# Performance work log

Hardware: AMD Instinct MI355X
Metric: run time of the kernel (lower is better)

The kernel has to match this reference:

```python
import jax, jax.numpy as jnp
import numpy as np
from jax.scipy.special import logsumexp

B, T, S, V = 64, 1024, 512, 1024


def setup_inputs() -> dict:
    key = jax.random.key(0)
    k_obs, k_emis, k_trans, k_prior = jax.random.split(key, 4)
    observations = jax.random.randint(k_obs, (B, T), 0, V, dtype=jnp.int32)
    emission_table = jax.random.normal(k_emis, (V, S), dtype=jnp.float32)
    transitions = jax.random.normal(k_trans, (S, S), dtype=jnp.float32)
    prior = jax.random.normal(k_prior, (S,), dtype=jnp.float32)
    return {
        "observations": observations,
        "emission_table": emission_table,
        "transitions": transitions,
        "prior": prior,
    }


def reference(observations, emission_table, transitions, prior):
    # alpha_0[b, s] = emission_logits(obs_0)[b, s] + prior[s]
    alpha0 = emission_table[observations[:, 0]] + prior  # [B, S]

    def step(alpha, obs_t):
        # new_alpha[b, j] = emis[b, j] + logsumexp_i(alpha[b, i] + trans[i, j])
        e = emission_table[obs_t]  # [B, S]
        a = e + logsumexp(alpha[:, :, None] + transitions[None, :, :], axis=1)
        return a, None

    # scan over time steps 1..T-1; xs is [T-1, B]
    alpha, _ = jax.lax.scan(step, alpha0, observations[:, 1:].T)
    return logsumexp(alpha, axis=1)  # [B]
```

## Files before the change

kernel.cpp:

```cpp
#include <hip/hip_runtime.h>


constexpr int Bn = 64, Tn = 1024, Sn = 512;
#define L2E 1.44269504f

typedef int v4i __attribute__((ext_vector_type(4)));

#if __has_builtin(__builtin_amdgcn_update_dpp)
template <int CTRL>
__device__ __forceinline__ float dpp_fmax(float x) {
    int s = __builtin_bit_cast(int, x);
    int d = __builtin_amdgcn_update_dpp(s, s, CTRL, 0xf, 0xf, false);
    return fmaxf(x, __builtin_bit_cast(float, d));
}
__device__ __forceinline__ float wave_max64(float x) {
    x = dpp_fmax<0x121>(x);
    x = dpp_fmax<0x122>(x);
    x = dpp_fmax<0x124>(x);
    x = dpp_fmax<0x128>(x);
    x = dpp_fmax<0x142>(x);
    x = dpp_fmax<0x143>(x);
    return __builtin_bit_cast(float,
        __builtin_amdgcn_readlane(__builtin_bit_cast(int, x), 63));
}
__device__ __forceinline__ float max_of_8_pattern(float x) {
    x = dpp_fmax<0x121>(x);
    x = dpp_fmax<0x122>(x);
    x = dpp_fmax<0x124>(x);
    return x;
}
#else
__device__ __forceinline__ float wave_max64(float x) {
    #pragma unroll
    for (int off = 32; off; off >>= 1) x = fmaxf(x, __shfl_xor(x, off, 64));
    return x;
}
__device__ __forceinline__ float max_of_8_pattern(float x) {
    #pragma unroll
    for (int off = 1; off < 8; off <<= 1) x = fmaxf(x, __shfl_xor(x, off, 64));
    return x;
}
#endif

__device__ __forceinline__ int bfrag_addr(int i, int c) {
    return ((((c >> 4) * 8 + (i >> 6)) * 64) + ((i >> 4) & 3) * 16 + (c & 15)) * 16
           + (i & 15);
}

__global__ __launch_bounds__(256) void prep_rows(
    const float* __restrict__ trans, unsigned char* __restrict__ EqB,
    float* __restrict__ rowmax)
{
    const int i = blockIdx.x;
    const int j = threadIdx.x;
    const int lane = j & 63, wv = j >> 6;
    float t0 = trans[i * Sn + j];
    float t1 = trans[i * Sn + j + 256];
    float m = fmaxf(t0, t1);
    #pragma unroll
    for (int off = 32; off; off >>= 1) m = fmaxf(m, __shfl_xor(m, off, 64));
    __shared__ float rm[4];
    if (lane == 0) rm[wv] = m;
    __syncthreads();
    m = fmaxf(fmaxf(rm[0], rm[1]), fmaxf(rm[2], rm[3]));
    if (j == 0) rowmax[i] = m;
    int q0 = __float2int_rn(127.f * __expf(t0 - m));
    int q1 = __float2int_rn(127.f * __expf(t1 - m));
    EqB[bfrag_addr(i, j)] = (unsigned char)q0;
    EqB[bfrag_addr(i, j + 256)] = (unsigned char)q1;
}

__global__ __launch_bounds__(512) void prep_scale(
    const float* __restrict__ rowmax, float* __restrict__ lr,
    float* __restrict__ Cp)
{
    const int i = threadIdx.x;
    const int lane = i & 63, wv = i >> 6;
    float m = rowmax[i];
    float rm = m;
    #pragma unroll
    for (int off = 32; off; off >>= 1) rm = fmaxf(rm, __shfl_xor(rm, off, 64));
    __shared__ float red[8];
    if (lane == 0) red[wv] = rm;
    __syncthreads();
    float RM = red[0];
    #pragma unroll
    for (int w = 1; w < 8; ++w) RM = fmaxf(RM, red[w]);
    lr[i] = (m - RM) * L2E + 6.98868469f;
    if (i == 0) *Cp = RM - 9.68837417f;
}

__global__ __launch_bounds__(512, 2) void hmm_fwd(
    const int* __restrict__ obs,
    const float* __restrict__ emis,
    const float* __restrict__ prior,
    const v4i* __restrict__ EqB4,
    const float* __restrict__ lr,
    const float* __restrict__ Cp,
    float* __restrict__ out)
{
    const int b = blockIdx.x;
    const int tid = threadIdx.x;
    const int lane = tid & 63, wv = tid >> 6;
    const int q = lane >> 4;

    __shared__ int obs_s[Tn];
    __shared__ __align__(16) unsigned char Pq[2][Sn];
    __shared__ float redm[2][8];
    __shared__ float reds[8];

    obs_s[tid] = obs[b * Tn + tid];
    obs_s[tid + 512] = obs[b * Tn + 512 + tid];

    v4i Bf[4][8];
    #pragma unroll
    for (int tau = 0; tau < 4; ++tau)
        #pragma unroll
        for (int kap = 0; kap < 8; ++kap)
            Bf[tau][kap] = EqB4[((wv * 4 + tau) * 8 + kap) * 64 + lane];

    const float lr_t = lr[tid];
    const float C = *Cp;

    __syncthreads();

    float a = emis[obs_s[0] * Sn + tid] + prior[tid];
    float e_next = emis[obs_s[1] * Sn + tid];

    for (int t = 1; t < Tn; ++t) {
        const int pb = t & 1;

        float mw = wave_max64(a);
        if (lane == 0) redm[pb][wv] = mw;
        __syncthreads();
        float m = max_of_8_pattern(redm[pb][lane & 7]);

        int gi = __float2int_rn(exp2f(fmaf(a - m, L2E, lr_t)));
        Pq[pb][tid] = (unsigned char)gi;
        __syncthreads();

        float e_cur = e_next;
        if (t < Tn - 1) e_next = emis[obs_s[t + 1] * Sn + tid];

        const unsigned char* Pbase = Pq[pb] + q * 16;
        v4i Af[8];
        #pragma unroll
        for (int kap = 0; kap < 8; ++kap)
            Af[kap] = *(const v4i*)(Pbase + kap * 64);

        v4i acc[4];
        #pragma unroll
        for (int tau = 0; tau < 4; ++tau) {
            v4i z = {0, 0, 0, 0};
            #pragma unroll
            for (int kap = 0; kap < 8; ++kap)
                z = __builtin_amdgcn_mfma_i32_16x16x64_i8(Af[kap], Bf[tau][kap],
                                                          z, 0, 0, 0);
            acc[tau] = z;
        }

        int idot = (lane < 16) ? acc[0].x
                 : (lane < 32) ? acc[1].x
                 : (lane < 48) ? acc[2].x
                               : acc[3].x;

        a = e_cur + m + C + __logf((float)idot);
    }

    float m = a;
    #pragma unroll
    for (int off = 32; off; off >>= 1) m = fmaxf(m, __shfl_xor(m, off, 64));
    if (lane == 0) redm[0][wv] = m;
    __syncthreads();
    #pragma unroll
    for (int w = 0; w < 8; ++w) m = fmaxf(m, redm[0][w]);

    float s = __expf(a - m);
    #pragma unroll
    for (int off = 32; off; off >>= 1) s += __shfl_xor(s, off, 64);
    if (lane == 0) reds[wv] = s;
    __syncthreads();
    if (tid == 0) {
        float tot = 0.f;
        #pragma unroll
        for (int w = 0; w < 8; ++w) tot += reds[w];
        out[b] = m + __logf(tot);
    }
}

extern "C" void kernel_launch(void* const* d_in, const int* in_sizes, int n_in,
                              void* d_out, int out_size, void* d_ws, size_t ws_size,
                              hipStream_t stream) {
    const int*   obs   = (const int*)d_in[0];
    const float* emis  = (const float*)d_in[1];
    const float* trans = (const float*)d_in[2];
    const float* prior = (const float*)d_in[3];
    float* out = (float*)d_out;

    unsigned char* EqB = (unsigned char*)d_ws;
    float* rowmax = (float*)(EqB + Sn * Sn);
    float* lr     = rowmax + Sn;
    float* Cp     = lr + Sn;

    prep_rows<<<Sn, 256, 0, stream>>>(trans, EqB, rowmax);
    prep_scale<<<1, Sn, 0, stream>>>(rowmax, lr, Cp);
    hmm_fwd<<<Bn, Sn, 0, stream>>>(obs, emis, prior,
                                   (const v4i*)EqB, lr, Cp, out);
}
```

Measured before the change: 1.011 ms.

## Quantize per-wave with local max, drop one barrier per step, rescale per K-chunk

Each wave now quantizes its alpha slice against its own wave max instead of the block-wide max, so the first barrier that waited for the global max is removed. The per-wave maxima are read after the single remaining barrier, and each K-chunk's integer MFMA partial (one chunk per wave's 64 states) is rescaled by exp(wave_max - global_max) in float before summing. This cuts one __syncthreads per time step on the serial recurrence. In exchange it issues each MFMA with a zero accumulator, adding per-chunk int-to-float conversions, lane selects and FMAs, plus eight exp2 per step.

Result: slower. 1.252 ms (+23.8%).

```diff
diff --git a/kernel.cpp b/kernel.cpp
--- a/kernel.cpp
+++ b/kernel.cpp
@@ -23,21 +23,10 @@
     return __builtin_bit_cast(float,
         __builtin_amdgcn_readlane(__builtin_bit_cast(int, x), 63));
 }
-__device__ __forceinline__ float max_of_8_pattern(float x) {
-    x = dpp_fmax<0x121>(x);
-    x = dpp_fmax<0x122>(x);
-    x = dpp_fmax<0x124>(x);
-    return x;
-}
 #else
 __device__ __forceinline__ float wave_max64(float x) {
     #pragma unroll
     for (int off = 32; off; off >>= 1) x = fmaxf(x, __shfl_xor(x, off, 64));
-    return x;
-}
-__device__ __forceinline__ float max_of_8_pattern(float x) {
-    #pragma unroll
-    for (int off = 1; off < 8; off <<= 1) x = fmaxf(x, __shfl_xor(x, off, 64));
     return x;
 }
 #endif
@@ -106,7 +95,7 @@
 
     __shared__ int obs_s[Tn];
     __shared__ __align__(16) unsigned char Pq[2][Sn];
-    __shared__ float redm[2][8];
+    __shared__ __align__(16) float redm[2][8];
     __shared__ float reds[8];
 
     obs_s[tid] = obs[b * Tn + tid];
@@ -131,40 +120,52 @@
         const int pb = t & 1;
 
         float mw = wave_max64(a);
+
+        int gi = __float2int_rn(exp2f(fmaf(a - mw, L2E, lr_t)));
+        Pq[pb][tid] = (unsigned char)gi;
         if (lane == 0) redm[pb][wv] = mw;
         __syncthreads();
-        float m = max_of_8_pattern(redm[pb][lane & 7]);
-
-        int gi = __float2int_rn(exp2f(fmaf(a - m, L2E, lr_t)));
-        Pq[pb][tid] = (unsigned char)gi;
-        __syncthreads();
 
         float e_cur = e_next;
         if (t < Tn - 1) e_next = emis[obs_s[t + 1] * Sn + tid];
 
+        float4 r0 = *(const float4*)&redm[pb][0];
+        float4 r1 = *(const float4*)&redm[pb][4];
+
         const unsigned char* Pbase = Pq[pb] + q * 16;
         v4i Af[8];
         #pragma unroll
         for (int kap = 0; kap < 8; ++kap)
             Af[kap] = *(const v4i*)(Pbase + kap * 64);
 
-        v4i acc[4];
-        #pragma unroll
-        for (int tau = 0; tau < 4; ++tau) {
-            v4i z = {0, 0, 0, 0};
-            #pragma unroll
-            for (int kap = 0; kap < 8; ++kap)
-                z = __builtin_amdgcn_mfma_i32_16x16x64_i8(Af[kap], Bf[tau][kap],
-                                                          z, 0, 0, 0);
-            acc[tau] = z;
+        float m = fmaxf(fmaxf(fmaxf(r0.x, r0.y), fmaxf(r0.z, r0.w)),
+                        fmaxf(fmaxf(r1.x, r1.y), fmaxf(r1.z, r1.w)));
+        float w[8];
+        w[0] = exp2f((r0.x - m) * L2E);
+        w[1] = exp2f((r0.y - m) * L2E);
+        w[2] = exp2f((r0.z - m) * L2E);
+        w[3] = exp2f((r0.w - m) * L2E);
+        w[4] = exp2f((r1.x - m) * L2E);
+        w[5] = exp2f((r1.y - m) * L2E);
+        w[6] = exp2f((r1.z - m) * L2E);
+        w[7] = exp2f((r1.w - m) * L2E);
+
+        float fdot = 0.f;
+        #pragma unroll
+        for (int kap = 0; kap < 8; ++kap) {
+            const v4i zz = {0, 0, 0, 0};
+            v4i z0 = __builtin_amdgcn_mfma_i32_16x16x64_i8(Af[kap], Bf[0][kap], zz, 0, 0, 0);
+            v4i z1 = __builtin_amdgcn_mfma_i32_16x16x64_i8(Af[kap], Bf[1][kap], zz, 0, 0, 0);
+            v4i z2 = __builtin_amdgcn_mfma_i32_16x16x64_i8(Af[kap], Bf[2][kap], zz, 0, 0, 0);
+            v4i z3 = __builtin_amdgcn_mfma_i32_16x16x64_i8(Af[kap], Bf[3][kap], zz, 0, 0, 0);
+            int sel = (lane < 16) ? z0.x
+                    : (lane < 32) ? z1.x
+                    : (lane < 48) ? z2.x
+                                  : z3.x;
+            fdot = fmaf(w[kap], (float)sel, fdot);
         }
 
-        int idot = (lane < 16) ? acc[0].x
-                 : (lane < 32) ? acc[1].x
-                 : (lane < 48) ? acc[2].x
-                               : acc[3].x;
-
-        a = e_cur + m + C + __logf((float)idot);
+        a = e_cur + (m + C) + __logf(fdot);
     }
 
     float m = a;
```
